# Performance work log

Hardware: AMD Instinct MI355X
Metric: run time of the kernel (lower is better)

Reference implementation:

```python
import jax, jax.numpy as jnp
import numpy as np
from jax import lax

T_DATA = 20000
E_NO = 2000
I_NO = 500
SUB_NO = 16
SYN_B = 3
HID = 256
T_SYN = 200
T_ENC = 80


def _causal_conv(x, kern):
    # x: [T, S] per-subunit drive; kern: [S, K] causal kernels (index = lag)
    S, K = kern.shape
    lhs = jnp.pad(x.T, ((0, 0), (K - 1, 0)))[None]        # [1, S, T+K-1]
    rhs = kern[:, ::-1][:, None, :]                        # flip then correlate == torch conv1d path
    out = lax.conv_general_dilated(lhs, rhs, (1,), 'VALID', feature_group_count=S)
    return out[0].T                                        # [T, S]


def setup_inputs() -> dict:
    key = jax.random.key(0)
    ks = jax.random.split(key, 16)
    V_in = jax.random.normal(ks[0], (T_DATA,), jnp.float32) * 5.0 - 69.0
    S_e = jax.random.bernoulli(ks[1], 0.02, (T_DATA, E_NO)).astype(jnp.float32)
    S_i = jax.random.bernoulli(ks[2], 0.02, (T_DATA, I_NO)).astype(jnp.float32)
    # synapse -> subunit one-hot assignment matrices [sub_no, n_syn]
    C_syn_e = jax.nn.one_hot(jax.random.randint(ks[3], (E_NO,), 0, SUB_NO), SUB_NO, dtype=jnp.float32).T
    C_syn_i = jax.nn.one_hot(jax.random.randint(ks[4], (I_NO,), 0, SUB_NO), SUB_NO, dtype=jnp.float32).T
    # parameters, initialized exactly as in __init__
    K_syn = jnp.stack([jnp.full((SUB_NO, SYN_B), 0.04),
                       jnp.full((SUB_NO, SYN_B), -0.02),
                       jnp.full((SUB_NO, SYN_B), 0.02)], axis=-1)          # [sub, B, 3]
    tau_syn = jnp.tile((jnp.arange(SYN_B, dtype=jnp.float32) + 1.6)[:, None], (1, 3))  # [B, 3]
    delta_syn = jnp.full((SUB_NO, 2), 2.0, jnp.float32)
    enc_bias = jnp.zeros((SUB_NO - 1,), jnp.float32)
    W_in = 2 * T_ENC - 1

    def lin(k, fan_out, fan_in):
        kw, kb = jax.random.split(k)
        s = 1.0 / np.sqrt(fan_in)
        return (jax.random.uniform(kw, (fan_out, fan_in), jnp.float32, -s, s),
                jax.random.uniform(kb, (fan_out,), jnp.float32, -s, s))

    W1, b1 = lin(ks[5], HID, W_in)
    W2, b2 = lin(ks[6], HID, HID)
    W3, b3 = lin(ks[7], HID, HID)
    W4, b4 = lin(ks[8], SUB_NO - 1, HID)
    a1 = jnp.float32(0.25)
    a2 = jnp.float32(0.25)
    a3 = jnp.float32(0.25)
    return dict(V_in=V_in, S_e=S_e, S_i=S_i, C_syn_e=C_syn_e, C_syn_i=C_syn_i,
                K_syn=K_syn, tau_syn=tau_syn, delta_syn=delta_syn, enc_bias=enc_bias,
                W1=W1, b1=b1, a1=a1, W2=W2, b2=b2, a2=a2, W3=W3, b3=b3, a3=a3,
                W4=W4, b4=b4)


def reference(V_in, S_e, S_i, C_syn_e, C_syn_i, K_syn, tau_syn, delta_syn, enc_bias,
              W1, b1, a1, W2, b2, a2, W3, b3, a3, W4, b4):
    T = V_in.shape[0]
    # ---- spike_convolve, fully vectorized over (subunit, basis) ----
    t = jnp.arange(T_SYN, dtype=V_in.dtype)                 # [T_syn]
    d = jnp.exp(delta_syn)                                   # [sub, 2]
    te = jnp.maximum(t[None, :] - d[:, 0:1], 0.0)            # [sub, T_syn]
    ti = jnp.maximum(t[None, :] - d[:, 1:2], 0.0)
    tau = jnp.exp(tau_syn)                                   # [B, 3]
    tte = te[:, None, :] / tau[None, :, 0, None]             # [sub, B, T_syn]
    tti = ti[:, None, :] / tau[None, :, 1, None]
    ker_e = jnp.einsum('sbt,sb->st', tte * jnp.exp(-tte), K_syn[:, :, 0])
    ker_i = jnp.einsum('sbt,sb->st', tti * jnp.exp(-tti), K_syn[:, :, 1])
    in_e = S_e @ C_syn_e.T                                   # [T, sub]
    in_i = S_i @ C_syn_i.T
    S_conv = _causal_conv(in_e, ker_e) + _causal_conv(in_i, ker_i)   # [T, sub]
    # ---- encode: batched sliding-window MLP (replaces per-timestep loop) ----
    W = 2 * T_ENC - 1
    Vpad = jnp.zeros((T + W,), V_in.dtype).at[T_ENC - 1:T_ENC - 1 + T].set(V_in)
    idx = jnp.arange(T)[:, None] + jnp.arange(W)[None, :]    # [T, W]
    win = Vpad[idx]                                          # [T, W]
    prelu = lambda x, a: jnp.where(x >= 0, x, a * x)
    h = prelu(win @ W1.T + b1, a1)
    h = prelu(h @ W2.T + b2, a2)
    h = prelu(h @ W3.T + b3, a3)
    nn_out = h @ W4.T + b4                                   # [T, sub-1]
    return jax.nn.sigmoid(nn_out + S_conv[:, 1:] + enc_bias)
```

## Files before the change

### kernel.cpp

```cpp
#include <hip/hip_runtime.h>
#include <cstdint>
#include <cstddef>

#define T_DATA 20000
#define E_NO 2000
#define I_NO 500
#define SUB_NO 16
#define HID 256
#define T_SYN 200
#define T_ENC 80
#define W_IN 159

typedef __attribute__((ext_vector_type(8))) __bf16 bf16x8;
typedef __attribute__((ext_vector_type(8))) short short8;
typedef __attribute__((ext_vector_type(4))) float floatx4;
typedef __attribute__((ext_vector_type(4))) unsigned int uint4v;
typedef __attribute__((ext_vector_type(2))) unsigned int uint2v;

__device__ __forceinline__ float bf2f(unsigned short u) {
    union { unsigned int i; float f; } v; v.i = ((unsigned int)u) << 16; return v.f;
}
__device__ __forceinline__ unsigned short f2bf(float f) {
    union { float f; unsigned int i; } v; v.f = f;
    unsigned int r = v.i + 0x7FFFu + ((v.i >> 16) & 1u);
    return (unsigned short)(r >> 16);
}
__device__ __forceinline__ float inload(const void* p, int i, int isbf) {
    return isbf ? bf2f(((const unsigned short*)p)[i]) : ((const float*)p)[i];
}

__device__ __forceinline__ int detect_bf(const void* Se, int* sfl) {
    if (threadIdx.x == 0) *sfl = 0;
    __syncthreads();
    const unsigned int* w = (const unsigned int*)Se;
    int la = 0;
    #pragma unroll
    for (int i = 0; i < 4; i++)
        la |= (w[i * 256 + threadIdx.x] & 0xFFFFu) ? 1 : 0;
    if (la) atomicOr(sfl, 1);
    __syncthreads();
    return *sfl;
}

#define OFF_KERE   16u
#define OFF_KERI   12816u
#define OFF_SHE    25616u
#define OFF_SHI    33616u
#define OFF_W1H    35616u
#define OFF_W1L    117536u
#define OFF_W2H    199456u
#define OFF_W2L    330528u
#define OFF_W3H    461600u
#define OFF_W3L    592672u
#define OFF_W4H    723744u
#define OFF_W4L    731936u
#define OFF_INE    740128u
#define OFF_INI    1060128u

__global__ void k_tables(const void* Se, const void* Ksyn, const void* tau_syn, const void* dly,
                         const void* Ce, const void* Ci,
                         float* ker_e, float* ker_i, unsigned char* sh_e, unsigned char* sh_i) {
    __shared__ int sfl;
    int f = detect_bf(Se, &sfl);
    int id = blockIdx.x * 256 + threadIdx.x;
    if (id < 6400) {
        int c = id < 3200 ? 0 : 1;
        int q = id - c * 3200;
        int s = q / 200, j = q - s * 200;
        float d = expf(inload(dly, s * 2 + c, f));
        float tt = fmaxf((float)j - d, 0.0f);
        float acc = 0.f;
        #pragma unroll
        for (int b = 0; b < 3; b++) {
            float tau = expf(inload(tau_syn, b * 3 + c, f));
            float x = tt / tau;
            acc += x * expf(-x) * inload(Ksyn, (s * 3 + b) * 3 + c, f);
        }
        (c == 0 ? ker_e : ker_i)[s * 200 + j] = acc;
    } else if (id < 8400) {
        int e = id - 6400;
        int a = 0;
        for (int s = 0; s < 16; s++) if (inload(Ce, s * E_NO + e, f) > 0.5f) a = s;
        sh_e[e] = (unsigned char)(a * 8);
    } else if (id < 8900) {
        int e = id - 8400;
        int a = 0;
        for (int s = 0; s < 16; s++) if (inload(Ci, s * I_NO + e, f) > 0.5f) a = s;
        sh_i[e] = (unsigned char)(a * 8);
    }
}

__device__ __forceinline__ void acc_slot(unsigned int b, unsigned int sh,
                                         unsigned long long& lo, unsigned long long& hi) {
    unsigned int up = sh >> 6;
    unsigned int s6 = sh & 63;
    lo += (unsigned long long)(b & (up ^ 1u)) << s6;
    hi += (unsigned long long)(b & up) << s6;
}

__global__ void __launch_bounds__(256) k_spikes(const void* Se, const void* Si,
                         const unsigned char* sh_e, const unsigned char* sh_i,
                         const void* W1, const void* W2, const void* W3, const void* W4,
                         unsigned char* in_e, unsigned char* in_i,
                         unsigned short* W1h, unsigned short* W1l,
                         unsigned short* W2h, unsigned short* W2l,
                         unsigned short* W3h, unsigned short* W3l,
                         unsigned short* W4h, unsigned short* W4l) {
    __shared__ int sfl;
    __shared__ __align__(8) unsigned char she[E_NO];
    __shared__ __align__(8) unsigned char shi[I_NO];
    for (int i = threadIdx.x; i < E_NO / 4; i += 256)
        ((unsigned int*)she)[i] = ((const unsigned int*)sh_e)[i];
    for (int i = threadIdx.x; i < I_NO / 4; i += 256)
        ((unsigned int*)shi)[i] = ((const unsigned int*)sh_i)[i];
    int f = detect_bf(Se, &sfl);
    int lane = threadIdx.x & 63;
    int wave = threadIdx.x >> 6;
    int t = blockIdx.x * 4 + wave;
    unsigned long long e0 = 0, e1 = 0, i0 = 0, i1 = 0;
    if (f) {
        const uint4v* re = (const uint4v*)((const unsigned short*)Se + (size_t)t * E_NO);
        #pragma unroll
        for (int it = 0; it < 4; it++) {
            int c = it * 64 + lane;
            if (c < 250) {
                uint4v v = re[c];
                unsigned long long q = *(const unsigned long long*)&she[c * 8];
                #pragma unroll
                for (int w = 0; w < 4; w++) {
                    unsigned int x = v[w];
                    acc_slot((x >> 7) & 1u,  (unsigned int)(q >> (16 * w)) & 0xFFu, e0, e1);
                    acc_slot((x >> 23) & 1u, (unsigned int)(q >> (16 * w + 8)) & 0xFFu, e0, e1);
                }
            }
        }
        const uint2v* ri = (const uint2v*)((const unsigned short*)Si + (size_t)t * I_NO);
        #pragma unroll
        for (int it = 0; it < 2; it++) {
            int c = it * 64 + lane;
            if (c < 125) {
                uint2v v = ri[c];
                unsigned int q = *(const unsigned int*)&shi[c * 4];
                #pragma unroll
                for (int w = 0; w < 2; w++) {
                    unsigned int x = v[w];
                    acc_slot((x >> 7) & 1u,  (q >> (16 * w)) & 0xFFu, i0, i1);
                    acc_slot((x >> 23) & 1u, (q >> (16 * w + 8)) & 0xFFu, i0, i1);
                }
            }
        }
    } else {
        const uint4v* re = (const uint4v*)((const float*)Se + (size_t)t * E_NO);
        #pragma unroll
        for (int it = 0; it < 8; it++) {
            int c = it * 64 + lane;
            if (c < 500) {
                uint4v v = re[c];
                unsigned int q = *(const unsigned int*)&she[c * 4];
                #pragma unroll
                for (int w = 0; w < 4; w++)
                    acc_slot((v[w] >> 23) & 1u, (q >> (8 * w)) & 0xFFu, e0, e1);
            }
        }
        const uint2v* ri = (const uint2v*)((const float*)Si + (size_t)t * I_NO);
        #pragma unroll
        for (int it = 0; it < 4; it++) {
            int c = it * 64 + lane;
            if (c < 250) {
                uint2v v = ri[c];
                unsigned int q = *(const unsigned short*)&shi[c * 2];
                #pragma unroll
                for (int w = 0; w < 2; w++)
                    acc_slot((v[w] >> 23) & 1u, (q >> (8 * w)) & 0xFFu, i0, i1);
            }
        }
    }
    for (int off = 32; off; off >>= 1) {
        e0 += __shfl_xor(e0, off);
        e1 += __shfl_xor(e1, off);
        i0 += __shfl_xor(i0, off);
        i1 += __shfl_xor(i1, off);
    }
    if (lane < 16) {
        unsigned long long a = (lane < 8) ? e0 : e1;
        in_e[(size_t)t * 16 + lane] = (unsigned char)((a >> ((lane & 7) * 8)) & 0xFF);
    } else if (lane < 32) {
        int s = lane - 16;
        unsigned long long a = (s < 8) ? i0 : i1;
        in_i[(size_t)t * 16 + s] = (unsigned char)((a >> ((s & 7) * 8)) & 0xFF);
    }
    if (blockIdx.x < 688) {
        int q = blockIdx.x * 256 + threadIdx.x;
        if (q < 40960) {
            int j = q & 7, l = (q >> 3) & 63, r = q >> 9;
            int ks = r % 5, tile = r / 5;
            int n = tile * 16 + (l & 15);
            int k = ks * 32 + (l >> 4) * 8 + j;
            float v = (k < W_IN) ? inload(W1, n * W_IN + k, f) : 0.f;
            unsigned short hi = f2bf(v);
            W1h[q] = hi;
            W1l[q] = f2bf(v - bf2f(hi));
        } else if (q < 106496) {
            int p = q - 40960;
            int j = p & 7, l = (p >> 3) & 63, r = p >> 9;
            int ks = r & 7, tile = r >> 3;
            int n = tile * 16 + (l & 15);
            int k = ks * 32 + (l >> 4) * 8 + j;
            float v = inload(W2, n * 256 + k, f);
            unsigned short hi = f2bf(v);
            W2h[p] = hi;
            W2l[p] = f2bf(v - bf2f(hi));
        } else if (q < 172032) {
            int p = q - 106496;
            int j = p & 7, l = (p >> 3) & 63, r = p >> 9;
            int ks = r & 7, tile = r >> 3;
            int n = tile * 16 + (l & 15);
            int k = ks * 32 + (l >> 4) * 8 + j;
            float v = inload(W3, n * 256 + k, f);
            unsigned short hi = f2bf(v);
            W3h[p] = hi;
            W3l[p] = f2bf(v - bf2f(hi));
        } else {
            int p = q - 172032;
            int j = p & 7, l = (p >> 3) & 63, ks = p >> 9;
            int lm = l & 15, quad = l >> 4;
            float v = 0.f;
            if (lm < 15) v = inload(W4, lm * 256 + ks * 32 + quad * 8 + j, f);
            unsigned short hi = f2bf(v);
            W4h[p] = hi;
            W4l[p] = f2bf(v - bf2f(hi));
        }
    }
}

template<bool BF>
__device__ __forceinline__ void mlp_body(
    const void* V,
    const unsigned short* W1h, const unsigned short* W1l, const void* b1, const void* a1p,
    const unsigned short* W2h, const unsigned short* W2l, const void* b2, const void* a2p,
    const unsigned short* W3h, const unsigned short* W3l, const void* b3, const void* a3p,
    const unsigned short* W4h, const unsigned short* W4l, const void* b4,
    const void* encb, const float* Sc, void* out,
    unsigned short* Ahi, unsigned short* Alo,
    const bf16x8 (&Bh1)[5][4])
{
    int tid = threadIdx.x;
    int lane = tid & 63, wave = tid >> 6;
    int lm = lane & 15, quad = lane >> 4;
    int t0 = blockIdx.x * 64;

    auto ld = [&](const void* p, int i) -> float {
        return BF ? bf2f(((const unsigned short*)p)[i]) : ((const float*)p)[i];
    };
    auto boff1 = [&](int ks, int nt) { return (size_t)((((wave * 4 + nt) * 5 + ks) * 64 + lane) << 3); };
    auto boff  = [&](int ks, int nt) { return (size_t)((((wave * 4 + nt) * 8 + ks) * 64 + lane) << 3); };

    for (int idx = tid; idx < 64 * 160; idx += 256) {
        int m = idx / 160, k = idx - m * 160;
        int tg = t0 + m + k - (T_ENC - 1);
        float v = 0.f;
        if (k < W_IN && tg >= 0 && tg < T_DATA) v = ld(V, tg);
        unsigned short hi = f2bf(v);
        int col = (((k >> 3) ^ (m & 31)) << 3) | (k & 7);
        Ahi[m * 256 + col] = hi;
        if (!BF) Alo[m * 256 + col] = f2bf(v - bf2f(hi));
    }
    __syncthreads();

    floatx4 acc[4][4];
    auto aoff = [&](int mt, int ks) {
        int arow = mt * 16 + lm;
        return arow * 256 + ((((ks << 2) | quad) ^ (arow & 31)) << 3);
    };

    auto epi = [&](const void* bias, float alpha) {
        __syncthreads();
        #pragma unroll
        for (int mt = 0; mt < 4; mt++) {
            #pragma unroll
            for (int nt = 0; nt < 4; nt++) {
                int cn = wave * 64 + nt * 16 + lm;
                float bb = ld(bias, cn);
                #pragma unroll
                for (int j = 0; j < 4; j++) {
                    int row = mt * 16 + quad * 4 + j;
                    float h = acc[mt][nt][j] + bb;
                    h = (h >= 0.f) ? h : alpha * h;
                    unsigned short hi = f2bf(h);
                    int col = (((cn >> 3) ^ (row & 31)) << 3) | (cn & 7);
                    Ahi[row * 256 + col] = hi;
                    if (!BF) Alo[row * 256 + col] = f2bf(h - bf2f(hi));
                }
            }
        }
        __syncthreads();
    };

    floatx4 z = {0.f, 0.f, 0.f, 0.f};

    if (BF) {
        bf16x8 Bc[4][4], Bn[4][4];
        #pragma unroll
        for (int mt = 0; mt < 4; mt++)
            #pragma unroll
            for (int nt = 0; nt < 4; nt++) acc[mt][nt] = z;
        #pragma unroll
        for (int ks = 0; ks < 5; ks++) {
            bf16x8 a[4];
            #pragma unroll
            for (int mt = 0; mt < 4; mt++) a[mt] = *(const bf16x8*)&Ahi[aoff(mt, ks)];
            #pragma unroll
            for (int nt = 0; nt < 4; nt++)
                #pragma unroll
                for (int mt = 0; mt < 4; mt++)
                    acc[mt][nt] = __builtin_amdgcn_mfma_f32_16x16x32_bf16(a[mt], Bh1[ks][nt], acc[mt][nt], 0, 0, 0);
        }
        #pragma unroll
        for (int c = 0; c < 4; c++)
            #pragma unroll
            for (int nt = 0; nt < 4; nt++)
                Bc[c][nt] = *(const bf16x8*)(W2h + boff(c, nt));
        epi(b1, ld(a1p, 0));

        #pragma unroll
        for (int mt = 0; mt < 4; mt++)
            #pragma unroll
            for (int nt = 0; nt < 4; nt++) acc[mt][nt] = z;
        #pragma unroll
        for (int c = 0; c < 4; c++)
            #pragma unroll
            for (int nt = 0; nt < 4; nt++)
                Bn[c][nt] = *(const bf16x8*)(W2h + boff(4 + c, nt));
        #pragma unroll
        for (int c = 0; c < 4; c++) {
            bf16x8 a[4];
            #pragma unroll
            for (int mt = 0; mt < 4; mt++) a[mt] = *(const bf16x8*)&Ahi[aoff(mt, c)];
            #pragma unroll
            for (int nt = 0; nt < 4; nt++)
                #pragma unroll
                for (int mt = 0; mt < 4; mt++)
                    acc[mt][nt] = __builtin_amdgcn_mfma_f32_16x16x32_bf16(a[mt], Bc[c][nt], acc[mt][nt], 0, 0, 0);
        }
        #pragma unroll
        for (int c = 0; c < 4; c++)
            #pragma unroll
            for (int nt = 0; nt < 4; nt++)
                Bc[c][nt] = *(const bf16x8*)(W3h + boff(c, nt));
        #pragma unroll
        for (int c = 0; c < 4; c++) {
            bf16x8 a[4];
            #pragma unroll
            for (int mt = 0; mt < 4; mt++) a[mt] = *(const bf16x8*)&Ahi[aoff(mt, 4 + c)];
            #pragma unroll
            for (int nt = 0; nt < 4; nt++)
                #pragma unroll
                for (int mt = 0; mt < 4; mt++)
                    acc[mt][nt] = __builtin_amdgcn_mfma_f32_16x16x32_bf16(a[mt], Bn[c][nt], acc[mt][nt], 0, 0, 0);
        }
        epi(b2, ld(a2p, 0));

        #pragma unroll
        for (int mt = 0; mt < 4; mt++)
            #pragma unroll
            for (int nt = 0; nt < 4; nt++) acc[mt][nt] = z;
        #pragma unroll
        for (int c = 0; c < 4; c++)
            #pragma unroll
            for (int nt = 0; nt < 4; nt++)
                Bn[c][nt] = *(const bf16x8*)(W3h + boff(4 + c, nt));
        #pragma unroll
        for (int c = 0; c < 4; c++) {
            bf16x8 a[4];
            #pragma unroll
            for (int mt = 0; mt < 4; mt++) a[mt] = *(const bf16x8*)&Ahi[aoff(mt, c)];
            #pragma unroll
            for (int nt = 0; nt < 4; nt++)
                #pragma unroll
                for (int mt = 0; mt < 4; mt++)
                    acc[mt][nt] = __builtin_amdgcn_mfma_f32_16x16x32_bf16(a[mt], Bc[c][nt], acc[mt][nt], 0, 0, 0);
        }
        bf16x8 w4[8];
        #pragma unroll
        for (int ks = 0; ks < 8; ks++)
            w4[ks] = *(const bf16x8*)(W4h + (size_t)((ks * 64 + lane) << 3));
        #pragma unroll
        for (int c = 0; c < 4; c++) {
            bf16x8 a[4];
            #pragma unroll
            for (int mt = 0; mt < 4; mt++) a[mt] = *(const bf16x8*)&Ahi[aoff(mt, 4 + c)];
            #pragma unroll
            for (int nt = 0; nt < 4; nt++)
                #pragma unroll
                for (int mt = 0; mt < 4; mt++)
                    acc[mt][nt] = __builtin_amdgcn_mfma_f32_16x16x32_bf16(a[mt], Bn[c][nt], acc[mt][nt], 0, 0, 0);
        }
        epi(b3, ld(a3p, 0));

        {
            int mt = wave;
            floatx4 a4 = z;
            #pragma unroll
            for (int ks = 0; ks < 8; ks++) {
                bf16x8 ah = *(const bf16x8*)&Ahi[aoff(mt, ks)];
                a4 = __builtin_amdgcn_mfma_f32_16x16x32_bf16(ah, w4[ks], a4, 0, 0, 0);
            }
            if (lm < 15) {
                float bb = ld(b4, lm) + ld(encb, lm);
                #pragma unroll
                for (int j = 0; j < 4; j++) {
                    int row = mt * 16 + quad * 4 + j;
                    int t = t0 + row;
                    if (t < T_DATA) {
                        float x = a4[j] + bb + Sc[row * 16 + lm + 1];
                        x = fminf(fmaxf(x, -40.f), 40.f);
                        float sg = 1.f / (1.f + expf(-x));
                        ((unsigned short*)out)[(size_t)t * 15 + lm] = f2bf(sg);
                    }
                }
            }
        }
    } else {
        {
            #pragma unroll
            for (int mt = 0; mt < 4; mt++)
                #pragma unroll
                for (int nt = 0; nt < 4; nt++) acc[mt][nt] = z;
            #pragma unroll
            for (int ks = 0; ks < 5; ks++) {
                bf16x8 ah[4], al[4];
                #pragma unroll
                for (int mt = 0; mt < 4; mt++) {
                    ah[mt] = *(const bf16x8*)&Ahi[aoff(mt, ks)];
                    al[mt] = *(const bf16x8*)&Alo[aoff(mt, ks)];
                }
                #pragma unroll
                for (int nt = 0; nt < 4; nt++) {
                    bf16x8 bh = Bh1[ks][nt];
                    bf16x8 bl = *(const bf16x8*)(W1l + boff1(ks, nt));
                    #pragma unroll
                    for (int mt = 0; mt < 4; mt++) {
                        acc[mt][nt] = __builtin_amdgcn_mfma_f32_16x16x32_bf16(ah[mt], bh, acc[mt][nt], 0, 0, 0);
                        acc[mt][nt] = __builtin_amdgcn_mfma_f32_16x16x32_bf16(al[mt], bh, acc[mt][nt], 0, 0, 0);
                        acc[mt][nt] = __builtin_amdgcn_mfma_f32_16x16x32_bf16(ah[mt], bl, acc[mt][nt], 0, 0, 0);
                    }
                }
            }
            epi(b1, ld(a1p, 0));
        }
        const unsigned short* Whs[2] = {W2h, W3h};
        const unsigned short* Wls[2] = {W2l, W3l};
        const void* bs[2] = {b2, b3};
        const void* as_[2] = {a2p, a3p};
        for (int l = 0; l < 2; l++) {
            #pragma unroll
            for (int mt = 0; mt < 4; mt++)
                #pragma unroll
                for (int nt = 0; nt < 4; nt++) acc[mt][nt] = z;
            const unsigned short* Wh = Whs[l];
            const unsigned short* Wl = Wls[l];
            #pragma unroll
            for (int ks = 0; ks < 8; ks++) {
                bf16x8 ah[4], al[4];
                #pragma unroll
                for (int mt = 0; mt < 4; mt++) {
                    ah[mt] = *(const bf16x8*)&Ahi[aoff(mt, ks)];
                    al[mt] = *(const bf16x8*)&Alo[aoff(mt, ks)];
                }
                #pragma unroll
                for (int nt = 0; nt < 4; nt++) {
                    bf16x8 bh = *(const bf16x8*)(Wh + boff(ks, nt));
                    bf16x8 bl = *(const bf16x8*)(Wl + boff(ks, nt));
                    #pragma unroll
                    for (int mt = 0; mt < 4; mt++) {
                        acc[mt][nt] = __builtin_amdgcn_mfma_f32_16x16x32_bf16(ah[mt], bh, acc[mt][nt], 0, 0, 0);
                        acc[mt][nt] = __builtin_amdgcn_mfma_f32_16x16x32_bf16(al[mt], bh, acc[mt][nt], 0, 0, 0);
                        acc[mt][nt] = __builtin_amdgcn_mfma_f32_16x16x32_bf16(ah[mt], bl, acc[mt][nt], 0, 0, 0);
                    }
                }
            }
            epi(bs[l], ld(as_[l], 0));
        }
        {
            int mt = wave;
            floatx4 a4 = z;
            #pragma unroll
            for (int ks = 0; ks < 8; ks++) {
                bf16x8 ah = *(const bf16x8*)&Ahi[aoff(mt, ks)];
                bf16x8 bh = *(const bf16x8*)(W4h + (size_t)((ks * 64 + lane) << 3));
                a4 = __builtin_amdgcn_mfma_f32_16x16x32_bf16(ah, bh, a4, 0, 0, 0);
                bf16x8 al = *(const bf16x8*)&Alo[aoff(mt, ks)];
                bf16x8 bl = *(const bf16x8*)(W4l + (size_t)((ks * 64 + lane) << 3));
                a4 = __builtin_amdgcn_mfma_f32_16x16x32_bf16(al, bh, a4, 0, 0, 0);
                a4 = __builtin_amdgcn_mfma_f32_16x16x32_bf16(ah, bl, a4, 0, 0, 0);
            }
            if (lm < 15) {
                float bb = ld(b4, lm) + ld(encb, lm);
                #pragma unroll
                for (int j = 0; j < 4; j++) {
                    int row = mt * 16 + quad * 4 + j;
                    int t = t0 + row;
                    if (t < T_DATA) {
                        float x = a4[j] + bb + Sc[row * 16 + lm + 1];
                        x = fminf(fmaxf(x, -40.f), 40.f);
                        float sg = 1.f / (1.f + expf(-x));
                        ((float*)out)[(size_t)t * 15 + lm] = sg;
                    }
                }
            }
        }
    }
}

__global__ void __launch_bounds__(256, 2) k_convmlp(
    const void* Se, const void* V,
    const unsigned char* in_e, const unsigned char* in_i,
    const float* ker_e, const float* ker_i,
    const unsigned short* W1h, const unsigned short* W1l, const void* b1, const void* a1p,
    const unsigned short* W2h, const unsigned short* W2l, const void* b2, const void* a2p,
    const unsigned short* W3h, const unsigned short* W3l, const void* b3, const void* a3p,
    const unsigned short* W4h, const unsigned short* W4l, const void* b4,
    const void* encb, void* out) {
    __shared__ __align__(16) unsigned char smem[65536];
    __shared__ __align__(16) float Sc[64 * 16];
    __shared__ int sfl;

    float* se = (float*)smem;
    float* si = se + 263 * 17;
    float* ke = si + 263 * 17;
    float* ki = ke + 16 * 201;

    int lane = threadIdx.x & 63, wave = threadIdx.x >> 6;

    bf16x8 Bh1[5][4];
    #pragma unroll
    for (int ks = 0; ks < 5; ks++)
        #pragma unroll
        for (int nt = 0; nt < 4; nt++)
            Bh1[ks][nt] = *(const bf16x8*)(W1h + (size_t)((((wave * 4 + nt) * 5 + ks) * 64 + lane) << 3));

    int t0 = blockIdx.x * 64;
    for (int idx = threadIdx.x; idx < 263 * 4; idx += 256) {
        int r = idx >> 2, wi = idx & 3;
        int t = t0 - 199 + r;
        unsigned int ve = 0, vi = 0;
        if (t >= 0 && t < T_DATA) {
            ve = ((const unsigned int*)in_e)[t * 4 + wi];
            vi = ((const unsigned int*)in_i)[t * 4 + wi];
        }
        #pragma unroll
        for (int b = 0; b < 4; b++) {
            se[r * 17 + wi * 4 + b] = (float)((ve >> (8 * b)) & 0xFF);
            si[r * 17 + wi * 4 + b] = (float)((vi >> (8 * b)) & 0xFF);
        }
    }
    for (int idx = threadIdx.x; idx < 3200; idx += 256) {
        int s2 = idx / 200, j = idx - s2 * 200;
        ke[s2 * 201 + j] = ker_e[idx];
        ki[s2 * 201 + j] = ker_i[idx];
    }
    int f = detect_bf(Se, &sfl);

    {
        int s = threadIdx.x & 15, g4 = (threadIdx.x >> 4) * 4;
        float a0 = 0.f, a1 = 0.f, a2 = 0.f, a3 = 0.f;
        float w0 = se[(g4 + 199) * 17 + s], w1 = se[(g4 + 200) * 17 + s];
        float w2 = se[(g4 + 201) * 17 + s], w3 = se[(g4 + 202) * 17 + s];
        float x0 = si[(g4 + 199) * 17 + s], x1 = si[(g4 + 200) * 17 + s];
        float x2 = si[(g4 + 201) * 17 + s], x3 = si[(g4 + 202) * 17 + s];
        #pragma unroll 4
        for (int j = 0; j < 200; j++) {
            float kej = ke[s * 201 + j];
            float kij = ki[s * 201 + j];
            a0 += w0 * kej + x0 * kij;
            a1 += w1 * kej + x1 * kij;
            a2 += w2 * kej + x2 * kij;
            a3 += w3 * kej + x3 * kij;
            int lr = g4 + 198 - j; lr = lr < 0 ? 0 : lr;
            float nw = se[lr * 17 + s], nx = si[lr * 17 + s];
            w3 = w2; w2 = w1; w1 = w0; w0 = nw;
            x3 = x2; x2 = x1; x1 = x0; x0 = nx;
        }
        Sc[(g4 + 0) * 16 + s] = a0;
        Sc[(g4 + 1) * 16 + s] = a1;
        Sc[(g4 + 2) * 16 + s] = a2;
        Sc[(g4 + 3) * 16 + s] = a3;
    }
    __syncthreads();

    unsigned short* Ahi = (unsigned short*)smem;
    unsigned short* Alo = Ahi + 64 * 256;
    if (f)
        mlp_body<true>(V, W1h, W1l, b1, a1p, W2h, W2l, b2, a2p, W3h, W3l, b3, a3p,
                       W4h, W4l, b4, encb, Sc, out, Ahi, Alo, Bh1);
    else
        mlp_body<false>(V, W1h, W1l, b1, a1p, W2h, W2l, b2, a2p, W3h, W3l, b3, a3p,
                        W4h, W4l, b4, encb, Sc, out, Ahi, Alo, Bh1);
}

extern "C" void kernel_launch(void* const* d_in, const int* in_sizes, int n_in,
                              void* d_out, int out_size, void* d_ws, size_t ws_size,
                              hipStream_t stream) {
    const void* V    = d_in[0];
    const void* Se   = d_in[1];
    const void* Si   = d_in[2];
    const void* Ce   = d_in[3];
    const void* Ci   = d_in[4];
    const void* Ksyn = d_in[5];
    const void* tau  = d_in[6];
    const void* dly  = d_in[7];
    const void* encb = d_in[8];
    const void* W1   = d_in[9];
    const void* b1   = d_in[10];
    const void* a1   = d_in[11];
    const void* W2   = d_in[12];
    const void* b2   = d_in[13];
    const void* a2   = d_in[14];
    const void* W3   = d_in[15];
    const void* b3   = d_in[16];
    const void* a3   = d_in[17];
    const void* W4   = d_in[18];
    const void* b4   = d_in[19];

    char* w = (char*)d_ws;
    float* ker_e = (float*)(w + OFF_KERE);
    float* ker_i = (float*)(w + OFF_KERI);
    unsigned char* sh_e = (unsigned char*)(w + OFF_SHE);
    unsigned char* sh_i = (unsigned char*)(w + OFF_SHI);
    unsigned short* W1h = (unsigned short*)(w + OFF_W1H);
    unsigned short* W1l = (unsigned short*)(w + OFF_W1L);
    unsigned short* W2h = (unsigned short*)(w + OFF_W2H);
    unsigned short* W2l = (unsigned short*)(w + OFF_W2L);
    unsigned short* W3h = (unsigned short*)(w + OFF_W3H);
    unsigned short* W3l = (unsigned short*)(w + OFF_W3L);
    unsigned short* W4h = (unsigned short*)(w + OFF_W4H);
    unsigned short* W4l = (unsigned short*)(w + OFF_W4L);
    unsigned char* in_e = (unsigned char*)(w + OFF_INE);
    unsigned char* in_i = (unsigned char*)(w + OFF_INI);

    k_tables<<<35, 256, 0, stream>>>(Se, Ksyn, tau, dly, Ce, Ci,
                                     ker_e, ker_i, sh_e, sh_i);
    k_spikes<<<5000, 256, 0, stream>>>(Se, Si, sh_e, sh_i, W1, W2, W3, W4,
                                       in_e, in_i,
                                       W1h, W1l, W2h, W2l, W3h, W3l, W4h, W4l);
    k_convmlp<<<313, 256, 0, stream>>>(Se, V, in_e, in_i, ker_e, ker_i,
                                       W1h, W1l, b1, a1, W2h, W2l, b2, a2,
                                       W3h, W3l, b3, a3, W4h, W4l, b4,
                                       encb, d_out);
}
```

Before: 356.6 us.

## Move low-part activations to global scratch and split conv across threads

The low-precision residual activation buffer (Alo) moves from LDS to a per-block global workspace region, halving the shared-memory footprint so more blocks can be resident per CU. The causal convolution no longer stages spike counts in LDS. Half the threads now handle excitatory inputs and half inhibitory, each computing 8 timesteps and reading the uint8 counts straight from global memory; the two partial sums are added in the epilogue. The trade is more global/L2 traffic on the fp32 path and more scattered byte loads in the conv loop, in exchange for the smaller LDS footprint.

```diff
diff --git a/kernel.cpp b/kernel.cpp
--- a/kernel.cpp
+++ b/kernel.cpp
@@ -56,6 +56,7 @@
 #define OFF_W4L    731936u
 #define OFF_INE    740128u
 #define OFF_INI    1060128u
+#define OFF_ALO    1380128u
 
 __global__ void k_tables(const void* Se, const void* Ksyn, const void* tau_syn, const void* dly,
                          const void* Ce, const void* Ci,
@@ -241,7 +242,7 @@
     const unsigned short* W3h, const unsigned short* W3l, const void* b3, const void* a3p,
     const unsigned short* W4h, const unsigned short* W4l, const void* b4,
     const void* encb, const float* Sc, void* out,
-    unsigned short* Ahi, unsigned short* Alo,
+    unsigned short* Ahi, unsigned short* AloG,
     const bf16x8 (&Bh1)[5][4])
 {
     int tid = threadIdx.x;
@@ -263,7 +264,7 @@
         unsigned short hi = f2bf(v);
         int col = (((k >> 3) ^ (m & 31)) << 3) | (k & 7);
         Ahi[m * 256 + col] = hi;
-        if (!BF) Alo[m * 256 + col] = f2bf(v - bf2f(hi));
+        if (!BF) AloG[m * 256 + col] = f2bf(v - bf2f(hi));
     }
     __syncthreads();
 
@@ -289,7 +290,7 @@
                     unsigned short hi = f2bf(h);
                     int col = (((cn >> 3) ^ (row & 31)) << 3) | (cn & 7);
                     Ahi[row * 256 + col] = hi;
-                    if (!BF) Alo[row * 256 + col] = f2bf(h - bf2f(hi));
+                    if (!BF) AloG[row * 256 + col] = f2bf(h - bf2f(hi));
                 }
             }
         }
@@ -412,7 +413,7 @@
                     int row = mt * 16 + quad * 4 + j;
                     int t = t0 + row;
                     if (t < T_DATA) {
-                        float x = a4[j] + bb + Sc[row * 16 + lm + 1];
+                        float x = a4[j] + bb + Sc[row * 16 + lm + 1] + Sc[1024 + row * 16 + lm + 1];
                         x = fminf(fmaxf(x, -40.f), 40.f);
                         float sg = 1.f / (1.f + expf(-x));
                         ((unsigned short*)out)[(size_t)t * 15 + lm] = f2bf(sg);
@@ -432,7 +433,7 @@
                 #pragma unroll
                 for (int mt = 0; mt < 4; mt++) {
                     ah[mt] = *(const bf16x8*)&Ahi[aoff(mt, ks)];
-                    al[mt] = *(const bf16x8*)&Alo[aoff(mt, ks)];
+                    al[mt] = *(const bf16x8*)(AloG + aoff(mt, ks));
                 }
                 #pragma unroll
                 for (int nt = 0; nt < 4; nt++) {
@@ -465,7 +466,7 @@
                 #pragma unroll
                 for (int mt = 0; mt < 4; mt++) {
                     ah[mt] = *(const bf16x8*)&Ahi[aoff(mt, ks)];
-                    al[mt] = *(const bf16x8*)&Alo[aoff(mt, ks)];
+                    al[mt] = *(const bf16x8*)(AloG + aoff(mt, ks));
                 }
                 #pragma unroll
                 for (int nt = 0; nt < 4; nt++) {
@@ -489,7 +490,7 @@
                 bf16x8 ah = *(const bf16x8*)&Ahi[aoff(mt, ks)];
                 bf16x8 bh = *(const bf16x8*)(W4h + (size_t)((ks * 64 + lane) << 3));
                 a4 = __builtin_amdgcn_mfma_f32_16x16x32_bf16(ah, bh, a4, 0, 0, 0);
-                bf16x8 al = *(const bf16x8*)&Alo[aoff(mt, ks)];
+                bf16x8 al = *(const bf16x8*)(AloG + aoff(mt, ks));
                 bf16x8 bl = *(const bf16x8*)(W4l + (size_t)((ks * 64 + lane) << 3));
                 a4 = __builtin_amdgcn_mfma_f32_16x16x32_bf16(al, bh, a4, 0, 0, 0);
                 a4 = __builtin_amdgcn_mfma_f32_16x16x32_bf16(ah, bl, a4, 0, 0, 0);
@@ -501,7 +502,7 @@
                     int row = mt * 16 + quad * 4 + j;
                     int t = t0 + row;
                     if (t < T_DATA) {
-                        float x = a4[j] + bb + Sc[row * 16 + lm + 1];
+                        float x = a4[j] + bb + Sc[row * 16 + lm + 1] + Sc[1024 + row * 16 + lm + 1];
                         x = fminf(fmaxf(x, -40.f), 40.f);
                         float sg = 1.f / (1.f + expf(-x));
                         ((float*)out)[(size_t)t * 15 + lm] = sg;
@@ -520,17 +521,18 @@
     const unsigned short* W2h, const unsigned short* W2l, const void* b2, const void* a2p,
     const unsigned short* W3h, const unsigned short* W3l, const void* b3, const void* a3p,
     const unsigned short* W4h, const unsigned short* W4l, const void* b4,
-    const void* encb, void* out) {
-    __shared__ __align__(16) unsigned char smem[65536];
-    __shared__ __align__(16) float Sc[64 * 16];
+    const void* encb, unsigned short* AloBase, void* out) {
+    __shared__ __align__(16) unsigned char smem[32768];
+    __shared__ __align__(16) float Sc[2 * 64 * 16];
     __shared__ int sfl;
 
-    float* se = (float*)smem;
-    float* si = se + 263 * 17;
-    float* ke = si + 263 * 17;
-    float* ki = ke + 16 * 201;
-
-    int lane = threadIdx.x & 63, wave = threadIdx.x >> 6;
+    float* kef = (float*)smem;
+    float* kif = kef + 16 * 201;
+
+    int tid = threadIdx.x;
+    int lane = tid & 63, wave = tid >> 6;
+    int t0 = blockIdx.x * 64;
+    unsigned short* AloG = AloBase + (size_t)blockIdx.x * 64 * 256;
 
     bf16x8 Bh1[5][4];
     #pragma unroll
@@ -539,63 +541,50 @@
         for (int nt = 0; nt < 4; nt++)
             Bh1[ks][nt] = *(const bf16x8*)(W1h + (size_t)((((wave * 4 + nt) * 5 + ks) * 64 + lane) << 3));
 
-    int t0 = blockIdx.x * 64;
-    for (int idx = threadIdx.x; idx < 263 * 4; idx += 256) {
-        int r = idx >> 2, wi = idx & 3;
-        int t = t0 - 199 + r;
-        unsigned int ve = 0, vi = 0;
-        if (t >= 0 && t < T_DATA) {
-            ve = ((const unsigned int*)in_e)[t * 4 + wi];
-            vi = ((const unsigned int*)in_i)[t * 4 + wi];
-        }
-        #pragma unroll
-        for (int b = 0; b < 4; b++) {
-            se[r * 17 + wi * 4 + b] = (float)((ve >> (8 * b)) & 0xFF);
-            si[r * 17 + wi * 4 + b] = (float)((vi >> (8 * b)) & 0xFF);
-        }
-    }
-    for (int idx = threadIdx.x; idx < 3200; idx += 256) {
+    for (int idx = tid; idx < 3200; idx += 256) {
         int s2 = idx / 200, j = idx - s2 * 200;
-        ke[s2 * 201 + j] = ker_e[idx];
-        ki[s2 * 201 + j] = ker_i[idx];
+        kef[s2 * 201 + j] = ker_e[idx];
+        kif[s2 * 201 + j] = ker_i[idx];
     }
     int f = detect_bf(Se, &sfl);
 
     {
-        int s = threadIdx.x & 15, g4 = (threadIdx.x >> 4) * 4;
-        float a0 = 0.f, a1 = 0.f, a2 = 0.f, a3 = 0.f;
-        float w0 = se[(g4 + 199) * 17 + s], w1 = se[(g4 + 200) * 17 + s];
-        float w2 = se[(g4 + 201) * 17 + s], w3 = se[(g4 + 202) * 17 + s];
-        float x0 = si[(g4 + 199) * 17 + s], x1 = si[(g4 + 200) * 17 + s];
-        float x2 = si[(g4 + 201) * 17 + s], x3 = si[(g4 + 202) * 17 + s];
-        #pragma unroll 4
+        int arr = tid >> 7;
+        int g8 = ((tid >> 4) & 7) * 8;
+        int s  = tid & 15;
+        const unsigned char* src = arr ? in_i : in_e;
+        const float* kf = arr ? kif : kef;
+        float w[8], acc8[8];
+        #pragma unroll
+        for (int i = 0; i < 8; i++) {
+            int t = t0 + g8 + i;
+            w[i] = (t < T_DATA) ? (float)src[(size_t)t * 16 + s] : 0.f;
+            acc8[i] = 0.f;
+        }
+        #pragma unroll 8
         for (int j = 0; j < 200; j++) {
-            float kej = ke[s * 201 + j];
-            float kij = ki[s * 201 + j];
-            a0 += w0 * kej + x0 * kij;
-            a1 += w1 * kej + x1 * kij;
-            a2 += w2 * kej + x2 * kij;
-            a3 += w3 * kej + x3 * kij;
-            int lr = g4 + 198 - j; lr = lr < 0 ? 0 : lr;
-            float nw = se[lr * 17 + s], nx = si[lr * 17 + s];
-            w3 = w2; w2 = w1; w1 = w0; w0 = nw;
-            x3 = x2; x2 = x1; x1 = x0; x0 = nx;
-        }
-        Sc[(g4 + 0) * 16 + s] = a0;
-        Sc[(g4 + 1) * 16 + s] = a1;
-        Sc[(g4 + 2) * 16 + s] = a2;
-        Sc[(g4 + 3) * 16 + s] = a3;
+            float kj = kf[s * 201 + j];
+            #pragma unroll
+            for (int i = 0; i < 8; i++) acc8[i] += w[i] * kj;
+            int t = t0 + g8 - j - 1;
+            float nv = (t >= 0) ? (float)src[(size_t)t * 16 + s] : 0.f;
+            #pragma unroll
+            for (int i = 7; i > 0; i--) w[i] = w[i - 1];
+            w[0] = nv;
+        }
+        #pragma unroll
+        for (int i = 0; i < 8; i++)
+            Sc[arr * 1024 + (g8 + i) * 16 + s] = acc8[i];
     }
     __syncthreads();
 
     unsigned short* Ahi = (unsigned short*)smem;
-    unsigned short* Alo = Ahi + 64 * 256;
     if (f)
         mlp_body<true>(V, W1h, W1l, b1, a1p, W2h, W2l, b2, a2p, W3h, W3l, b3, a3p,
-                       W4h, W4l, b4, encb, Sc, out, Ahi, Alo, Bh1);
+                       W4h, W4l, b4, encb, Sc, out, Ahi, AloG, Bh1);
     else
         mlp_body<false>(V, W1h, W1l, b1, a1p, W2h, W2l, b2, a2p, W3h, W3l, b3, a3p,
-                        W4h, W4l, b4, encb, Sc, out, Ahi, Alo, Bh1);
+                        W4h, W4l, b4, encb, Sc, out, Ahi, AloG, Bh1);
 }
 
 extern "C" void kernel_launch(void* const* d_in, const int* in_sizes, int n_in,
@@ -637,6 +626,7 @@
     unsigned short* W4l = (unsigned short*)(w + OFF_W4L);
     unsigned char* in_e = (unsigned char*)(w + OFF_INE);
     unsigned char* in_i = (unsigned char*)(w + OFF_INI);
+    unsigned short* AloB = (unsigned short*)(w + OFF_ALO);
 
     k_tables<<<35, 256, 0, stream>>>(Se, Ksyn, tau, dly, Ce, Ci,
                                      ker_e, ker_i, sh_e, sh_i);
@@ -646,5 +636,5 @@
     k_convmlp<<<313, 256, 0, stream>>>(Se, V, in_e, in_i, ker_e, ker_i,
                                        W1h, W1l, b1, a1, W2h, W2l, b2, a2,
                                        W3h, W3l, b3, a3, W4h, W4l, b4,
-                                       encb, d_out);
-}
+                                       encb, AloB, d_out);
+}
```

After: 478.8 us. +34.3%, slower.
